# Performance work log

Hardware: AMD Instinct MI355X
Metric: run time of the kernel (lower is better)

The kernel has to match this reference:

```python
import jax, jax.numpy as jnp
import numpy as np

B, S, D_IN, D_OUT, H = 2, 2048, 1024, 1024, 16
HD = D_OUT // H

def setup_inputs() -> dict:
    key = jax.random.key(0)
    ks = jax.random.split(key, 6)
    sc = 1.0 / np.sqrt(D_IN)
    return {
        "x": jax.random.normal(ks[0], (B, S, D_IN), dtype=jnp.float32),
        "Wq": jax.random.normal(ks[1], (D_IN, D_OUT), dtype=jnp.float32) * sc,
        "Wk": jax.random.normal(ks[2], (D_IN, D_OUT), dtype=jnp.float32) * sc,
        "Wv": jax.random.normal(ks[3], (D_IN, D_OUT), dtype=jnp.float32) * sc,
        "Wo": jax.random.normal(ks[4], (D_OUT, D_OUT), dtype=jnp.float32) * (1.0 / np.sqrt(D_OUT)),
        "bo": jax.random.normal(ks[5], (D_OUT,), dtype=jnp.float32) * 0.01,
    }

def reference(x, Wq, Wk, Wv, Wo, bo):
    b, n, _ = x.shape
    # QKV projections -> [b, h, n, hd]
    def split_heads(t):
        return t.reshape(b, n, H, HD).transpose(0, 2, 1, 3)
    q = split_heads(x @ Wq)
    k = split_heads(x @ Wk)
    v = split_heads(x @ Wv)
    scores = jnp.einsum("bhqd,bhkd->bhqk", q, k) / jnp.sqrt(jnp.float32(HD))
    causal = jnp.tril(jnp.ones((n, n), dtype=bool))  # True = keep
    scores = jnp.where(causal[None, None], scores, -jnp.inf)
    attn = jax.nn.softmax(scores, axis=-1)
    ctx = jnp.einsum("bhqk,bhkd->bhqd", attn, v)  # [b,h,n,hd]
    ctx = ctx.transpose(0, 2, 1, 3).reshape(b, n, D_OUT)
    return ctx @ Wo + bo
```

## Files before the change

### kernel.cpp

```cpp
#include <hip/hip_runtime.h>

#define B_  2
#define S_  2048
#define D_  1024
#define H_  16
#define HD_ 64
#define M_  (B_*S_)

typedef __bf16 bf16_t;
typedef __bf16 bf16x8 __attribute__((ext_vector_type(8)));
typedef float  f32x4  __attribute__((ext_vector_type(4)));

union U16x8 { uint4 u; bf16x8 v; };
union U16x4 { uint2 u; bf16_t e[4]; };

__device__ __forceinline__ bf16x8 ld_frag(const bf16_t* p) {
    U16x8 t; t.u = *(const uint4*)p; return t.v;
}

__device__ __forceinline__ void gload16(const bf16_t* g, bf16_t* l) {
    __builtin_amdgcn_global_load_lds(
        (const __attribute__((address_space(1))) unsigned int*)g,
        (__attribute__((address_space(3))) unsigned int*)l,
        16, 0, 0);
}

__global__ __launch_bounds__(256) void cvt_x(const float* __restrict__ xin,
                                             bf16_t* __restrict__ xout) {
    int i = (blockIdx.x * 256 + threadIdx.x) * 8;
    float4 a = *(const float4*)(xin + i);
    float4 b = *(const float4*)(xin + i + 4);
    bf16_t o[8] = {(bf16_t)a.x, (bf16_t)a.y, (bf16_t)a.z, (bf16_t)a.w,
                   (bf16_t)b.x, (bf16_t)b.y, (bf16_t)b.z, (bf16_t)b.w};
    *(uint4*)(xout + i) = *(uint4*)o;
}

__global__ __launch_bounds__(256) void transpose_w4(const float* __restrict__ w0,
                                                    const float* __restrict__ w1,
                                                    const float* __restrict__ w2,
                                                    const float* __restrict__ w3,
                                                    bf16_t* __restrict__ outbase) {
    __shared__ bf16_t tile[32][33];
    const int RC = 1024;
    int z = blockIdx.z;
    const float* in = (z == 0) ? w0 : (z == 1) ? w1 : (z == 2) ? w2 : w3;
    bf16_t* out = outbase + (size_t)z * RC * RC;
    int c0 = blockIdx.x * 32, r0 = blockIdx.y * 32;
    int tx = threadIdx.x, ty = threadIdx.y;
#pragma unroll
    for (int i = 0; i < 32; i += 8)
        tile[ty + i][tx] = (bf16_t)in[(size_t)(r0 + ty + i) * RC + c0 + tx];
    __syncthreads();
#pragma unroll
    for (int i = 0; i < 32; i += 8)
        out[(size_t)(c0 + ty + i) * RC + r0 + tx] = tile[tx][ty + i];
}

#define GEMM_CORE(A_, Wt_)                                                    \
    const int K = 1024;                                                       \
    __shared__ __align__(16) bf16_t smem[32768];                              \
    int t = threadIdx.x;                                                      \
    int wid = t >> 6, lane = t & 63, ln = lane & 15, quad = lane >> 4;        \
    int wm = (wid >> 1) * 64, wn = (wid & 1) * 64;                            \
    f32x4 zero = {0.f, 0.f, 0.f, 0.f};                                        \
    f32x4 acc[4][4];                                                          \
    _Pragma("unroll") for (int i = 0; i < 4; i++)                             \
        _Pragma("unroll") for (int j = 0; j < 4; j++) acc[i][j] = zero;       \
    int sr8 = lane >> 3, sc8 = (lane & 7) * 8;                                \
    const size_t arow = (size_t)(m0 + sr8) * K + sc8;                         \
    const size_t brow = (size_t)(n0 + sr8) * K + sc8;                         \
    _Pragma("unroll") for (int c = 0; c < 4; c++) {                           \
        int rb = c * 32 + wid * 8;                                            \
        gload16(A_  + arow + (size_t)rb * K, smem + rb * 64);                 \
        gload16(Wt_ + brow + (size_t)rb * K, smem + 8192 + rb * 64);          \
    }                                                                         \
    __syncthreads();                                                          \
    int cur = 0;                                                              \
    for (int k0 = 0; k0 < K; k0 += 64) {                                      \
        bf16_t* a_lds = smem + cur * 16384;                                   \
        bf16_t* b_lds = a_lds + 8192;                                         \
        if (k0 + 64 < K) {                                                    \
            bf16_t* an = smem + (cur ^ 1) * 16384;                            \
            _Pragma("unroll") for (int c = 0; c < 4; c++) {                   \
                int rb = c * 32 + wid * 8;                                    \
                gload16(A_  + arow + (size_t)rb * K + k0 + 64, an + rb * 64); \
                gload16(Wt_ + brow + (size_t)rb * K + k0 + 64,                \
                        an + 8192 + rb * 64);                                 \
            }                                                                 \
        }                                                                     \
        _Pragma("unroll") for (int ks = 0; ks < 2; ks++) {                    \
            bf16x8 af[4], bfr[4];                                             \
            _Pragma("unroll") for (int i = 0; i < 4; i++)                     \
                af[i] = ld_frag(a_lds + (wm + i * 16 + ln) * 64 + ks * 32 + quad * 8); \
            _Pragma("unroll") for (int j = 0; j < 4; j++)                     \
                bfr[j] = ld_frag(b_lds + (wn + j * 16 + ln) * 64 + ks * 32 + quad * 8); \
            _Pragma("unroll") for (int i = 0; i < 4; i++)                     \
                _Pragma("unroll") for (int j = 0; j < 4; j++)                 \
                    acc[i][j] = __builtin_amdgcn_mfma_f32_16x16x32_bf16(      \
                        af[i], bfr[j], acc[i][j], 0, 0, 0);                   \
        }                                                                     \
        __syncthreads();                                                      \
        cur ^= 1;                                                             \
    }

__global__ __launch_bounds__(256) void gemm_qkv(const bf16_t* __restrict__ A,
                                                const bf16_t* __restrict__ wtbase,
                                                bf16_t* __restrict__ outbase) {
    int wsel = blockIdx.x >> 3;
    int n0 = (blockIdx.x & 7) * 128;
    int m0 = blockIdx.y * 128;
    const bf16_t* Wt = wtbase + (size_t)wsel * 1024 * 1024;
    bf16_t* out = outbase + (size_t)wsel * 4 * 1024 * 1024;

    GEMM_CORE(A, Wt)

    if (wsel < 2) {
#pragma unroll
        for (int i = 0; i < 4; i++)
#pragma unroll
            for (int j = 0; j < 4; j++) {
                int n = n0 + wn + j * 16 + ln;
                int h = n >> 6, hd = n & 63;
#pragma unroll
                for (int r = 0; r < 4; r++) {
                    int m = m0 + wm + i * 16 + quad * 4 + r;
                    int b = m >> 11, s = m & 2047;
                    out[(((size_t)(b * H_ + h) * S_ + s) * HD_) + hd] =
                        (bf16_t)acc[i][j][r];
                }
            }
    } else {
        bf16_t* tr = smem;
#pragma unroll
        for (int i = 0; i < 4; i++)
#pragma unroll
            for (int j = 0; j < 4; j++) {
                U16x4 pk;
#pragma unroll
                for (int r = 0; r < 4; r++) pk.e[r] = (bf16_t)acc[i][j][r];
                *(uint2*)(tr + (wn + j * 16 + ln) * 136 + wm + i * 16 + quad * 4) = pk.u;
            }
        __syncthreads();
        int row = t >> 1, half = t & 1;
        int n = n0 + row;
        int h = n >> 6, hd = n & 63;
        int b = m0 >> 11, s0 = (m0 & 2047) + half * 64;
        const bf16_t* src = tr + row * 136 + half * 64;
        bf16_t* dst = out + (((size_t)(b * H_ + h) * HD_ + hd) * S_) + s0;
#pragma unroll
        for (int u = 0; u < 8; u++)
            *(uint4*)(dst + u * 8) = *(const uint4*)(src + u * 8);
    }
}

__global__ __launch_bounds__(256) void gemm_out(const bf16_t* __restrict__ A,
                                                const bf16_t* __restrict__ Wt,
                                                float* __restrict__ out,
                                                const float* __restrict__ bias) {
    const int N = 1024;
    int n0 = blockIdx.x * 128;
    int m0 = blockIdx.y * 128;

    GEMM_CORE(A, Wt)

#pragma unroll
    for (int i = 0; i < 4; i++)
#pragma unroll
        for (int j = 0; j < 4; j++) {
            int n = n0 + wn + j * 16 + ln;
            float bv = bias[n];
#pragma unroll
            for (int r = 0; r < 4; r++) {
                int m = m0 + wm + i * 16 + quad * 4 + r;
                out[(size_t)m * N + n] = acc[i][j][r] + bv;
            }
        }
}

__global__ __launch_bounds__(256) void attn64(const bf16_t* __restrict__ Q,
                                              const bf16_t* __restrict__ Kg,
                                              const bf16_t* __restrict__ Vt,
                                              bf16_t* __restrict__ ctx) {
    __shared__ __align__(16) bf16_t k_lds[64 * 72];
    __shared__ __align__(16) bf16_t v_lds[64 * 72];
    __shared__ __align__(16) bf16_t p_lds[4 * 16 * 72];

    int t = threadIdx.x;
    int wid = t >> 6, lane = t & 63, ln = lane & 15, quad = lane >> 4;

    int bid = blockIdx.x;
    int xcd = bid & 7, slot = bid >> 3;
    int bh  = xcd + ((slot >> 4) << 3);
    int pair = slot & 15;
    int b = bh >> 4, h = bh & 15;
    const bf16_t* Qb = Q  + (size_t)bh * S_ * HD_;
    const bf16_t* Kb = Kg + (size_t)bh * S_ * HD_;
    const bf16_t* Vb = Vt + (size_t)bh * HD_ * S_;

    int srow = t >> 2, schunk = t & 3;
    bf16_t* plw = p_lds + wid * 16 * 72;
    f32x4 zero = {0.f, 0.f, 0.f, 0.f};

    for (int pass = 0; pass < 2; pass++) {
        int qt = pass ? (31 - pair) : pair;
        int q0 = qt * 64;
        int nkt = qt + 1;

        int qrow = q0 + wid * 16 + ln;
        bf16x8 qf0 = ld_frag(Qb + (size_t)qrow * HD_ + quad * 8);
        bf16x8 qf1 = ld_frag(Qb + (size_t)qrow * HD_ + 32 + quad * 8);

        f32x4 oacc[4];
#pragma unroll
        for (int i = 0; i < 4; i++) oacc[i] = zero;
        float lsum[4] = {0.f, 0.f, 0.f, 0.f};

        const uint4* ksrc = (const uint4*)(Kb + (size_t)srow * HD_);
        const uint4* vsrc = (const uint4*)(Vb + (size_t)srow * S_);
        uint4 kv0 = ksrc[schunk * 2], kv1 = ksrc[schunk * 2 + 1];
        uint4 vv0 = vsrc[schunk * 2], vv1 = vsrc[schunk * 2 + 1];

        for (int kt = 0; kt < nkt; kt++) {
            __syncthreads();
            *(uint4*)(k_lds + srow * 72 + schunk * 16)     = kv0;
            *(uint4*)(k_lds + srow * 72 + schunk * 16 + 8) = kv1;
            *(uint4*)(v_lds + srow * 72 + schunk * 16)     = vv0;
            *(uint4*)(v_lds + srow * 72 + schunk * 16 + 8) = vv1;
            __syncthreads();
            if (kt + 1 < nkt) {
                int k0n = (kt + 1) * 64;
                ksrc = (const uint4*)(Kb + (size_t)(k0n + srow) * HD_);
                vsrc = (const uint4*)(Vb + (size_t)srow * S_ + k0n);
                kv0 = ksrc[schunk * 2]; kv1 = ksrc[schunk * 2 + 1];
                vv0 = vsrc[schunk * 2]; vv1 = vsrc[schunk * 2 + 1];
            }

            f32x4 sacc[4];
#pragma unroll
            for (int tt = 0; tt < 4; tt++) sacc[tt] = zero;
#pragma unroll
            for (int tt = 0; tt < 4; tt++) {
                bf16x8 b0 = ld_frag(k_lds + (tt * 16 + ln) * 72 + quad * 8);
                bf16x8 b1 = ld_frag(k_lds + (tt * 16 + ln) * 72 + 32 + quad * 8);
                sacc[tt] = __builtin_amdgcn_mfma_f32_16x16x32_bf16(qf0, b0, sacc[tt], 0, 0, 0);
                sacc[tt] = __builtin_amdgcn_mfma_f32_16x16x32_bf16(qf1, b1, sacc[tt], 0, 0, 0);
            }

            bool diag = (kt * 64 + 63 > q0 + wid * 16);
#pragma unroll
            for (int r = 0; r < 4; r++) {
                int q = q0 + wid * 16 + quad * 4 + r;
#pragma unroll
                for (int tt = 0; tt < 4; tt++) {
                    int k = kt * 64 + tt * 16 + ln;
                    float pv = __expf(__builtin_fmaf((float)sacc[tt][r], 0.125f, -16.0f));
                    if (diag && k > q) pv = 0.f;
                    lsum[r] += pv;
                    plw[(quad * 4 + r) * 72 + tt * 16 + ln] = (bf16_t)pv;
                }
            }

            bf16x8 pa0 = ld_frag(plw + ln * 72 + quad * 8);
            bf16x8 pa1 = ld_frag(plw + ln * 72 + 32 + quad * 8);
#pragma unroll
            for (int th = 0; th < 4; th++) {
                bf16x8 vb0 = ld_frag(v_lds + (th * 16 + ln) * 72 + quad * 8);
                bf16x8 vb1 = ld_frag(v_lds + (th * 16 + ln) * 72 + 32 + quad * 8);
                oacc[th] = __builtin_amdgcn_mfma_f32_16x16x32_bf16(pa0, vb0, oacc[th], 0, 0, 0);
                oacc[th] = __builtin_amdgcn_mfma_f32_16x16x32_bf16(pa1, vb1, oacc[th], 0, 0, 0);
            }
        }

#pragma unroll
        for (int r = 0; r < 4; r++) {
#pragma unroll
            for (int m = 1; m < 16; m <<= 1)
                lsum[r] += __shfl_xor(lsum[r], m, 64);
        }

#pragma unroll
        for (int r = 0; r < 4; r++) {
            int q = q0 + wid * 16 + quad * 4 + r;
            float inv = 1.f / lsum[r];
#pragma unroll
            for (int th = 0; th < 4; th++) {
                int hd = h * 64 + th * 16 + ln;
                ctx[((size_t)(b * S_ + q)) * D_ + hd] = (bf16_t)(oacc[th][r] * inv);
            }
        }
    }
}

extern "C" void kernel_launch(void* const* d_in, const int* in_sizes, int n_in,
                              void* d_out, int out_size, void* d_ws, size_t ws_size,
                              hipStream_t stream) {
    const float* x  = (const float*)d_in[0];
    const float* bo = (const float*)d_in[5];
    float* out = (float*)d_out;

    bf16_t* ws = (bf16_t*)d_ws;
    const size_t MM = 1024 * 1024;
    bf16_t* xb  = ws;
    bf16_t* ctx = xb;
    bf16_t* wtq = xb + 4 * MM;
    bf16_t* wto = wtq + 3 * MM;
    bf16_t* qb  = wto + MM;
    bf16_t* kb  = qb + 4 * MM;
    bf16_t* vtb = kb + 4 * MM;

    cvt_x<<<2048, 256, 0, stream>>>(x, xb);
    transpose_w4<<<dim3(32, 32, 4), dim3(32, 8, 1), 0, stream>>>(
        (const float*)d_in[1], (const float*)d_in[2],
        (const float*)d_in[3], (const float*)d_in[4], wtq);

    gemm_qkv<<<dim3(24, 32, 1), 256, 0, stream>>>(xb, wtq, qb);

    attn64<<<512, 256, 0, stream>>>(qb, kb, vtb, ctx);

    gemm_out<<<dim3(8, 32, 1), 256, 0, stream>>>(ctx, wto, out, bo);
}
```

Measured before the change: 205.2 us.

## Merge input conversion kernels and restructure GEMM K-loop with explicit vmcnt waits

Merges the x fp32-to-bf16 conversion and the weight transpose into a single ingest launch, using an extra grid z-slice for x. Rewrites the GEMM mainloop so both LDS buffers are prefetched up front. Each iteration waits with s_waitcnt vmcnt(8) and a raw s_barrier instead of __syncthreads, then refills the buffer it just consumed after a second barrier. The goal is to drop one kernel launch and keep global-to-LDS loads in flight two tiles ahead. The hand-placed waitcnt and barriers are fragile, and each k-step now has two barriers.

Result: slower. 211.0 us (+2.8%).

```diff
diff --git a/kernel.cpp b/kernel.cpp
--- a/kernel.cpp
+++ b/kernel.cpp
@@ -25,26 +25,32 @@
         16, 0, 0);
 }
 
-__global__ __launch_bounds__(256) void cvt_x(const float* __restrict__ xin,
-                                             bf16_t* __restrict__ xout) {
-    int i = (blockIdx.x * 256 + threadIdx.x) * 8;
-    float4 a = *(const float4*)(xin + i);
-    float4 b = *(const float4*)(xin + i + 4);
-    bf16_t o[8] = {(bf16_t)a.x, (bf16_t)a.y, (bf16_t)a.z, (bf16_t)a.w,
-                   (bf16_t)b.x, (bf16_t)b.y, (bf16_t)b.z, (bf16_t)b.w};
-    *(uint4*)(xout + i) = *(uint4*)o;
-}
-
-__global__ __launch_bounds__(256) void transpose_w4(const float* __restrict__ w0,
-                                                    const float* __restrict__ w1,
-                                                    const float* __restrict__ w2,
-                                                    const float* __restrict__ w3,
-                                                    bf16_t* __restrict__ outbase) {
-    __shared__ bf16_t tile[32][33];
+__global__ __launch_bounds__(256) void ingest(const float* __restrict__ w0,
+                                              const float* __restrict__ w1,
+                                              const float* __restrict__ w2,
+                                              const float* __restrict__ w3,
+                                              const float* __restrict__ xin,
+                                              bf16_t* __restrict__ wtout,
+                                              bf16_t* __restrict__ xout) {
     const int RC = 1024;
     int z = blockIdx.z;
+    if (z == 4) {
+        int bid = blockIdx.y * 32 + blockIdx.x;
+        int t = threadIdx.y * 32 + threadIdx.x;
+        int i = bid * 4096 + t * 16;
+#pragma unroll
+        for (int g = 0; g < 2; g++) {
+            float4 a = *(const float4*)(xin + i + g * 8);
+            float4 b = *(const float4*)(xin + i + g * 8 + 4);
+            bf16_t o[8] = {(bf16_t)a.x, (bf16_t)a.y, (bf16_t)a.z, (bf16_t)a.w,
+                           (bf16_t)b.x, (bf16_t)b.y, (bf16_t)b.z, (bf16_t)b.w};
+            *(uint4*)(xout + i + g * 8) = *(uint4*)o;
+        }
+        return;
+    }
+    __shared__ bf16_t tile[32][33];
     const float* in = (z == 0) ? w0 : (z == 1) ? w1 : (z == 2) ? w2 : w3;
-    bf16_t* out = outbase + (size_t)z * RC * RC;
+    bf16_t* out = wtout + (size_t)z * RC * RC;
     int c0 = blockIdx.x * 32, r0 = blockIdx.y * 32;
     int tx = threadIdx.x, ty = threadIdx.y;
 #pragma unroll
@@ -55,6 +61,13 @@
     for (int i = 0; i < 32; i += 8)
         out[(size_t)(c0 + ty + i) * RC + r0 + tx] = tile[tx][ty + i];
 }
+
+#define STAGE_TILE(A_, Wt_, koff, buf)                                        \
+    _Pragma("unroll") for (int c = 0; c < 4; c++) {                           \
+        int rb = c * 32 + wid * 8;                                            \
+        gload16(A_  + arow + (size_t)rb * K + (koff), (buf) + rb * 64);       \
+        gload16(Wt_ + brow + (size_t)rb * K + (koff), (buf) + 8192 + rb * 64);\
+    }
 
 #define GEMM_CORE(A_, Wt_)                                                    \
     const int K = 1024;                                                       \
@@ -69,25 +82,15 @@
     int sr8 = lane >> 3, sc8 = (lane & 7) * 8;                                \
     const size_t arow = (size_t)(m0 + sr8) * K + sc8;                         \
     const size_t brow = (size_t)(n0 + sr8) * K + sc8;                         \
-    _Pragma("unroll") for (int c = 0; c < 4; c++) {                           \
-        int rb = c * 32 + wid * 8;                                            \
-        gload16(A_  + arow + (size_t)rb * K, smem + rb * 64);                 \
-        gload16(Wt_ + brow + (size_t)rb * K, smem + 8192 + rb * 64);          \
-    }                                                                         \
-    __syncthreads();                                                          \
-    int cur = 0;                                                              \
-    for (int k0 = 0; k0 < K; k0 += 64) {                                      \
-        bf16_t* a_lds = smem + cur * 16384;                                   \
+    STAGE_TILE(A_, Wt_, 0, smem)                                              \
+    STAGE_TILE(A_, Wt_, 64, smem + 16384)                                     \
+    for (int it = 0; it < 16; it++) {                                         \
+        if (it < 15) asm volatile("s_waitcnt vmcnt(8)" ::: "memory");         \
+        else         asm volatile("s_waitcnt vmcnt(0)" ::: "memory");         \
+        __builtin_amdgcn_sched_barrier(0);                                    \
+        __builtin_amdgcn_s_barrier();                                         \
+        bf16_t* a_lds = smem + (it & 1) * 16384;                              \
         bf16_t* b_lds = a_lds + 8192;                                         \
-        if (k0 + 64 < K) {                                                    \
-            bf16_t* an = smem + (cur ^ 1) * 16384;                            \
-            _Pragma("unroll") for (int c = 0; c < 4; c++) {                   \
-                int rb = c * 32 + wid * 8;                                    \
-                gload16(A_  + arow + (size_t)rb * K + k0 + 64, an + rb * 64); \
-                gload16(Wt_ + brow + (size_t)rb * K + k0 + 64,                \
-                        an + 8192 + rb * 64);                                 \
-            }                                                                 \
-        }                                                                     \
         _Pragma("unroll") for (int ks = 0; ks < 2; ks++) {                    \
             bf16x8 af[4], bfr[4];                                             \
             _Pragma("unroll") for (int i = 0; i < 4; i++)                     \
@@ -99,8 +102,14 @@
                     acc[i][j] = __builtin_amdgcn_mfma_f32_16x16x32_bf16(      \
                         af[i], bfr[j], acc[i][j], 0, 0, 0);                   \
         }                                                                     \
-        __syncthreads();                                                      \
-        cur ^= 1;                                                             \
+        asm volatile("s_waitcnt lgkmcnt(0)" ::: "memory");                    \
+        __builtin_amdgcn_sched_barrier(0);                                    \
+        __builtin_amdgcn_s_barrier();                                         \
+        if (it < 14) {                                                        \
+            int koff = (it + 2) * 64;                                         \
+            bf16_t* bufn = smem + (it & 1) * 16384;                           \
+            STAGE_TILE(A_, Wt_, koff, bufn)                                   \
+        }                                                                     \
     }
 
 __global__ __launch_bounds__(256) void gemm_qkv(const bf16_t* __restrict__ A,
@@ -308,10 +317,9 @@
     bf16_t* kb  = qb + 4 * MM;
     bf16_t* vtb = kb + 4 * MM;
 
-    cvt_x<<<2048, 256, 0, stream>>>(x, xb);
-    transpose_w4<<<dim3(32, 32, 4), dim3(32, 8, 1), 0, stream>>>(
+    ingest<<<dim3(32, 32, 5), dim3(32, 8, 1), 0, stream>>>(
         (const float*)d_in[1], (const float*)d_in[2],
-        (const float*)d_in[3], (const float*)d_in[4], wtq);
+        (const float*)d_in[3], (const float*)d_in[4], x, wtq, xb);
 
     gemm_qkv<<<dim3(24, 32, 1), 256, 0, stream>>>(xb, wtq, qb);
 
```
